# Kernel tuning notes

Measured on AMD Instinct MI355X. Metric: run time of the kernel, lower is better.

Reference implementation:

```python
import jax, jax.numpy as jnp
import numpy as np

N = 100000       # nodes
E = 800000       # edges (avg degree 8)
D_IN = 256
D_H = 128
K = 16           # cluster_num
LAMBDA1 = 1.0    # args.alphaH
LAMBDA2 = 0.5    # args.alphaO
GAMMA = 0.1      # args.step_size_gamma


def setup_inputs() -> dict:
    key = jax.random.key(0)
    ks = jax.random.split(key, 8)
    x = jax.random.normal(ks[0], (N, D_IN), jnp.float32)
    edge_index = jax.random.randint(ks[1], (2, E), 0, N, jnp.int32)
    # learned params (glorot-ish small init to keep Gram term numerically tame)
    W1 = jax.random.normal(ks[2], (D_IN, D_H), jnp.float32) * 0.002
    b1 = jnp.zeros((D_H,), jnp.float32)
    W2 = jax.random.normal(ks[3], (D_H, D_H), jnp.float32) * 0.01
    b2 = jnp.zeros((D_H,), jnp.float32)
    Wf = jax.random.normal(ks[4], (D_H, K), jnp.float32) * 0.05
    bf = jnp.zeros((K,), jnp.float32)
    return {"x": x, "edge_index": edge_index, "W1": W1, "b1": b1,
            "W2": W2, "b2": b2, "Wf": Wf, "bf": bf}


def _gcn_norm(edge_index, n):
    # add self loops, symmetric normalization D^-1/2 A D^-1/2 (PyG gcn_norm)
    loops = jnp.arange(n, dtype=edge_index.dtype)
    row = jnp.concatenate([edge_index[0], loops])   # source
    col = jnp.concatenate([edge_index[1], loops])   # target
    w = jnp.ones(row.shape[0], jnp.float32)
    deg = jax.ops.segment_sum(w, col, num_segments=n)
    dinv = jnp.where(deg > 0, jax.lax.rsqrt(jnp.maximum(deg, 1.0)), 0.0)
    return row, col, dinv[row] * w * dinv[col]


def _deprop_layer(x, W, b, row, col, w, n):
    x = x @ W                                               # lin (no bias)
    z = (1.0 - GAMMA * LAMBDA1 + GAMMA * LAMBDA2) * x
    # propagate: gather source features, scale by edge weight, scatter-add to target
    s = GAMMA * LAMBDA1 * jax.ops.segment_sum(w[:, None] * x[row], col, num_segments=n)
    # dense Gram correction: x @ (x^T x), d_h x d_h contraction
    t = GAMMA * LAMBDA2 * (x @ (x.T @ x))
    return jax.nn.relu(z + s - t + b)                       # bias add + ReLU


def reference(x, edge_index, W1, b1, W2, b2, Wf, bf):
    n = x.shape[0]
    row, col, w = _gcn_norm(edge_index, n)  # cached=True -> computed once, reused
    x = _deprop_layer(x, W1, b1, row, col, w, n)
    x = _deprop_layer(x, W2, b2, row, col, w, n)
    logits = x @ Wf + bf                    # fc; dropout is identity in eval mode
    return jax.nn.log_softmax(logits, axis=1)
```

## Files before the change

kernel.cpp:

```cpp
#include <hip/hip_runtime.h>

#define NNODES 100000
#define NEDGES 800000
#define DIN    256
#define DH     128
#define KCLS   16
#define SCAN_NBLK 98
#define GCH 64
#define GRAM_BLK 256

typedef unsigned short u16;
typedef short s16x8 __attribute__((ext_vector_type(8)));
typedef float f32x4 __attribute__((ext_vector_type(4)));

static constexpr float CZ = 0.95f;
static constexpr float CS = 0.10f;
static constexpr float CT = 0.05f;

__device__ __forceinline__ u16 f2b(float f) {
    unsigned u = __builtin_bit_cast(unsigned, f);
    return (u16)((u + 0x7FFFu + ((u >> 16) & 1u)) >> 16);
}
__device__ __forceinline__ float b2f(u16 b) {
    return __builtin_bit_cast(float, ((unsigned)b) << 16);
}
__device__ __forceinline__ s16x8 f2b8(float4 u0, float4 u1) {
    s16x8 v;
    v[0] = (short)f2b(u0.x); v[1] = (short)f2b(u0.y);
    v[2] = (short)f2b(u0.z); v[3] = (short)f2b(u0.w);
    v[4] = (short)f2b(u1.x); v[5] = (short)f2b(u1.y);
    v[6] = (short)f2b(u1.z); v[7] = (short)f2b(u1.w);
    return v;
}


__global__ __launch_bounds__(256) void zero_kernel(int* __restrict__ p) {
    int i = blockIdx.x * 256 + threadIdx.x;
    if (i < NNODES) p[i] = 0;
}

__global__ __launch_bounds__(256) void hist_kernel(const int* __restrict__ col, int* counts) {
    int i = blockIdx.x * 256 + threadIdx.x;
    if (i < NEDGES) atomicAdd(&counts[col[i]], 1);
}

__global__ __launch_bounds__(256) void dinv_kernel(const int* __restrict__ counts, float* dinv) {
    int i = blockIdx.x * 256 + threadIdx.x;
    if (i < NNODES) dinv[i] = rsqrtf((float)(counts[i] + 1));
}

__global__ __launch_bounds__(256) void scan1_kernel(const int* __restrict__ counts,
                                                    int* __restrict__ offsets, int* __restrict__ bsum) {
    __shared__ int ls[256];
    const int b = blockIdx.x, t = threadIdx.x;
    const int base = b * 1024 + t * 4;
    int v0 = (base + 0 < NNODES) ? counts[base + 0] : 0;
    int v1 = (base + 1 < NNODES) ? counts[base + 1] : 0;
    int v2 = (base + 2 < NNODES) ? counts[base + 2] : 0;
    int v3 = (base + 3 < NNODES) ? counts[base + 3] : 0;
    ls[t] = v0 + v1 + v2 + v3;
    __syncthreads();
    for (int off = 1; off < 256; off <<= 1) {
        int v = (t >= off) ? ls[t - off] : 0;
        __syncthreads();
        ls[t] += v;
        __syncthreads();
    }
    int excl = (t == 0) ? 0 : ls[t - 1];
    if (t == 255) bsum[b] = ls[255];
    if (base + 0 < NNODES) offsets[base + 0] = excl;
    if (base + 1 < NNODES) offsets[base + 1] = excl + v0;
    if (base + 2 < NNODES) offsets[base + 2] = excl + v0 + v1;
    if (base + 3 < NNODES) offsets[base + 3] = excl + v0 + v1 + v2;
}

__global__ __launch_bounds__(128) void scan2_kernel(int* bsum) {
    __shared__ int ls[128];
    const int t = threadIdx.x;
    int v = (t < SCAN_NBLK) ? bsum[t] : 0;
    ls[t] = v;
    __syncthreads();
    for (int off = 1; off < 128; off <<= 1) {
        int u = (t >= off) ? ls[t - off] : 0;
        __syncthreads();
        ls[t] += u;
        __syncthreads();
    }
    if (t < SCAN_NBLK) bsum[t] = ls[t] - v;
}

__global__ __launch_bounds__(256) void scan3_kernel(int* __restrict__ offsets, const int* __restrict__ bsum) {
    const int b = blockIdx.x, t = threadIdx.x;
    const int add = bsum[b];
    const int base = b * 1024 + t * 4;
    #pragma unroll
    for (int i = 0; i < 4; ++i)
        if (base + i < NNODES) offsets[base + i] += add;
    if (b == 0 && t == 0) offsets[NNODES] = NEDGES;
}

__global__ __launch_bounds__(256)
void fill_kernel(const int* __restrict__ row, const int* __restrict__ col,
                 const int* __restrict__ offsets, int* __restrict__ cursor,
                 int* __restrict__ eidx) {
    int e = blockIdx.x * 256 + threadIdx.x;
    if (e >= NEDGES) return;
    int c = col[e];
    int p = offsets[c] + atomicAdd(&cursor[c], 1);
    eidx[p] = row[e];
}


template<int KD>
__global__ __launch_bounds__(256)
void tr_w_kernel(const float* __restrict__ W, u16* __restrict__ Wt) {
    int idx = blockIdx.x * 256 + threadIdx.x;
    if (idx < 128 * KD) {
        int c = idx / KD, k = idx % KD;
        Wt[idx] = f2b(W[k * 128 + c]);
    }
}

template<int KD, int EPI, int AF, int WS>
__global__ __launch_bounds__(256, 4)
void mm_bt(const void* __restrict__ Avoid, const u16* __restrict__ Bt,
           u16* __restrict__ Out, const u16* __restrict__ Hb,
           const u16* __restrict__ Sb, const float* __restrict__ bias,
           const float* __restrict__ dinvp, u16* __restrict__ Hs,
           int nrows)
{
    __shared__ __align__(16) u16 as_[2][128 * 40];
    __shared__ __align__(16) u16 bs_[2][128 * 40];
    const int t = threadIdx.x;
    const int w = t >> 6, l = t & 63;
    const int l15 = l & 15, g = l >> 4;
    const int row0 = blockIdx.x * 128;

    const u16*   Ab = (const u16*)Avoid;
    const float* Af = (const float*)Avoid;

    const int sr = t >> 2, so = t & 3;
    int arow[2];
    arow[0] = min(row0 + sr,      nrows - 1);
    arow[1] = min(row0 + 64 + sr, nrows - 1);

    #pragma unroll
    for (int i = 0; i < 2; ++i) {
        s16x8 va;
        if (AF) {
            const float4* p = (const float4*)&Af[(size_t)arow[i] * KD + so * 8];
            va = f2b8(p[0], p[1]);
        } else {
            va = *(const s16x8*)&Ab[(size_t)arow[i] * KD + so * 8];
        }
        s16x8 vb = *(const s16x8*)&Bt[(size_t)(sr + i * 64) * KD + so * 8];
        *(s16x8*)&as_[0][(sr + i * 64) * 40 + so * 8] = va;
        *(s16x8*)&bs_[0][(sr + i * 64) * 40 + so * 8] = vb;
    }
    __syncthreads();

    f32x4 acc[2][8] = {};
    constexpr int NK = KD / 32;

    for (int kc = 0; kc < NK; ++kc) {
        const int buf = kc & 1;
        s16x8 va[2], vb[2];
        const bool pf = (kc + 1 < NK);
        if (pf) {
            const int k0 = (kc + 1) * 32;
            #pragma unroll
            for (int i = 0; i < 2; ++i) {
                if (AF) {
                    const float4* p = (const float4*)&Af[(size_t)arow[i] * KD + k0 + so * 8];
                    va[i] = f2b8(p[0], p[1]);
                } else {
                    va[i] = *(const s16x8*)&Ab[(size_t)arow[i] * KD + k0 + so * 8];
                }
                vb[i] = *(const s16x8*)&Bt[(size_t)(sr + i * 64) * KD + k0 + so * 8];
            }
        }
        s16x8 af0 = *(const s16x8*)&as_[buf][(w * 32 +      l15) * 40 + g * 8];
        s16x8 af1 = *(const s16x8*)&as_[buf][(w * 32 + 16 + l15) * 40 + g * 8];
        #pragma unroll
        for (int n = 0; n < 8; ++n) {
            s16x8 bfr = *(const s16x8*)&bs_[buf][(n * 16 + l15) * 40 + g * 8];
            acc[0][n] = __builtin_amdgcn_mfma_f32_16x16x32_bf16(af0, bfr, acc[0][n], 0, 0, 0);
            acc[1][n] = __builtin_amdgcn_mfma_f32_16x16x32_bf16(af1, bfr, acc[1][n], 0, 0, 0);
        }
        if (pf) {
            #pragma unroll
            for (int i = 0; i < 2; ++i) {
                *(s16x8*)&as_[buf ^ 1][(sr + i * 64) * 40 + so * 8] = va[i];
                *(s16x8*)&bs_[buf ^ 1][(sr + i * 64) * 40 + so * 8] = vb[i];
            }
        }
        __syncthreads();
    }

    float bv[8];
    if (EPI) {
        #pragma unroll
        for (int n = 0; n < 8; ++n) bv[n] = bias[n * 16 + l15];
    }
    #pragma unroll
    for (int m = 0; m < 2; ++m) {
        #pragma unroll
        for (int j = 0; j < 4; ++j) {
            int grow = row0 + w * 32 + m * 16 + g * 4 + j;
            if (grow < nrows) {
                size_t base = (size_t)grow * 128;
                float dv = WS ? dinvp[grow] : 0.f;
                #pragma unroll
                for (int n = 0; n < 8; ++n) {
                    int col = n * 16 + l15;
                    float v = acc[m][n][j];
                    if (EPI) {
                        float h = b2f(Hb[base + col]);
                        float s = b2f(Sb[base + col]);
                        v = fmaxf(CZ * h + CS * s - CT * v + bv[n], 0.f);
                    }
                    Out[base + col] = f2b(v);
                    if (WS) Hs[base + col] = f2b(dv * v);
                }
            }
        }
    }
}

__global__ __launch_bounds__(256)
void gram_gather(const u16* __restrict__ Hb, const u16* __restrict__ Hsb,
                 const float* __restrict__ dinv,
                 const int* __restrict__ offsets, const int* __restrict__ eidx,
                 float* __restrict__ P, u16* __restrict__ Sb, int nrows)
{
    __shared__ __align__(16) u16 ht[128 * GCH];
    const int t = threadIdx.x;

    if (blockIdx.x < GRAM_BLK) {
        const int bid = blockIdx.x;
        const int w = t >> 6, l = t & 63;
        const int l15 = l & 15, g = l >> 4;
        const int nch = (nrows + GCH - 1) / GCH;

        f32x4 acc[2][8] = {};
        const int sr = t >> 2, sq = t & 3;

        for (int ch = bid; ch < nch; ch += GRAM_BLK) {
            {
                int gr = ch * GCH + sr;
                #pragma unroll
                for (int i4 = 0; i4 < 4; ++i4) {
                    int c0 = sq * 32 + i4 * 8;
                    s16x8 v = {};
                    if (gr < nrows) v = *(const s16x8*)&Hb[(size_t)gr * DH + c0];
                    #pragma unroll
                    for (int i = 0; i < 8; ++i) {
                        int c = c0 + i;
                        ht[c * GCH + (sr ^ ((c & 7) << 3))] = (u16)v[i];
                    }
                }
            }
            __syncthreads();
            #pragma unroll
            for (int ks = 0; ks < 2; ++ks) {
                const int kx = (ks * 32 + g * 8) ^ ((l & 7) << 3);
                s16x8 a0 = *(const s16x8*)&ht[(w * 32 +      l15) * GCH + kx];
                s16x8 a1 = *(const s16x8*)&ht[(w * 32 + 16 + l15) * GCH + kx];
                #pragma unroll
                for (int n = 0; n < 8; ++n) {
                    s16x8 bfr = *(const s16x8*)&ht[(n * 16 + l15) * GCH + kx];
                    acc[0][n] = __builtin_amdgcn_mfma_f32_16x16x32_bf16(a0, bfr, acc[0][n], 0, 0, 0);
                    acc[1][n] = __builtin_amdgcn_mfma_f32_16x16x32_bf16(a1, bfr, acc[1][n], 0, 0, 0);
                }
            }
            __syncthreads();
        }

        float* Pb = P + (size_t)bid * (DH * DH);
        #pragma unroll
        for (int m = 0; m < 2; ++m)
            #pragma unroll
            for (int j = 0; j < 4; ++j) {
                int prow = w * 32 + m * 16 + g * 4 + j;
                #pragma unroll
                for (int n = 0; n < 8; ++n)
                    Pb[prow * DH + n * 16 + l15] = acc[m][n][j];
            }
    } else {
        const int grp = t >> 4;
        const int gl  = t & 15;
        const int node = (blockIdx.x - GRAM_BLK) * 16 + grp;
        if (node >= NNODES) return;
        const s16x8* Hs8 = (const s16x8*)Hsb;
        const float d = dinv[node];
        s16x8 hv = Hs8[(size_t)node * 16 + gl];
        float a[8];
        #pragma unroll
        for (int i = 0; i < 8; ++i) a[i] = b2f((u16)hv[i]);
        int p = offsets[node];
        const int e = offsets[node + 1];
        for (; p + 3 < e; p += 4) {
            int r0 = eidx[p], r1 = eidx[p + 1], r2 = eidx[p + 2], r3 = eidx[p + 3];
            s16x8 h0 = Hs8[(size_t)r0 * 16 + gl];
            s16x8 h1 = Hs8[(size_t)r1 * 16 + gl];
            s16x8 h2 = Hs8[(size_t)r2 * 16 + gl];
            s16x8 h3 = Hs8[(size_t)r3 * 16 + gl];
            #pragma unroll
            for (int i = 0; i < 8; ++i) a[i] += b2f((u16)h0[i]);
            #pragma unroll
            for (int i = 0; i < 8; ++i) a[i] += b2f((u16)h1[i]);
            #pragma unroll
            for (int i = 0; i < 8; ++i) a[i] += b2f((u16)h2[i]);
            #pragma unroll
            for (int i = 0; i < 8; ++i) a[i] += b2f((u16)h3[i]);
        }
        for (; p < e; ++p) {
            int r0 = eidx[p];
            s16x8 h0 = Hs8[(size_t)r0 * 16 + gl];
            #pragma unroll
            for (int i = 0; i < 8; ++i) a[i] += b2f((u16)h0[i]);
        }
        s16x8 o;
        #pragma unroll
        for (int i = 0; i < 8; ++i) o[i] = (short)f2b(d * a[i]);
        ((s16x8*)Sb)[(size_t)node * 16 + gl] = o;
    }
}

__global__ __launch_bounds__(256)
void gram_reduce(const float* __restrict__ P, u16* __restrict__ Gb) {
    int idx = blockIdx.x * 256 + threadIdx.x;
    float s = 0.f;
    #pragma unroll 8
    for (int p = 0; p < GRAM_BLK; ++p)
        s += P[(size_t)p * (DH * DH) + idx];
    Gb[idx] = f2b(s);
}

__global__ __launch_bounds__(256)
void fc_mfma(const u16* __restrict__ Xb, const float* __restrict__ Wf,
             const float* __restrict__ bf, float* __restrict__ out, int nrows)
{
    __shared__ __align__(16) u16 wt[KCLS * DH];
    const int t = threadIdx.x;
    const int w = t >> 6, l = t & 63;
    const int l15 = l & 15, g = l >> 4;
    const int row0 = blockIdx.x * 128 + w * 32;

    for (int idx = t; idx < KCLS * DH; idx += 256) {
        int c = idx >> 7, k = idx & 127;
        wt[c * DH + (k ^ ((c & 7) << 3))] = f2b(Wf[k * KCLS + c]);
    }
    __syncthreads();

    int r[2];
    r[0] = min(row0 + l15,      nrows - 1);
    r[1] = min(row0 + 16 + l15, nrows - 1);

    f32x4 acc[2] = {};
    #pragma unroll
    for (int k0 = 0; k0 < DH; k0 += 32) {
        s16x8 a0 = *(const s16x8*)&Xb[(size_t)r[0] * DH + k0 + g * 8];
        s16x8 a1 = *(const s16x8*)&Xb[(size_t)r[1] * DH + k0 + g * 8];
        s16x8 bfr = *(const s16x8*)&wt[l15 * DH + ((k0 + g * 8) ^ ((l & 7) << 3))];
        acc[0] = __builtin_amdgcn_mfma_f32_16x16x32_bf16(a0, bfr, acc[0], 0, 0, 0);
        acc[1] = __builtin_amdgcn_mfma_f32_16x16x32_bf16(a1, bfr, acc[1], 0, 0, 0);
    }

    const float bias = bf[l15];
    #pragma unroll
    for (int m = 0; m < 2; ++m) {
        #pragma unroll
        for (int j = 0; j < 4; ++j) {
            int grow = row0 + m * 16 + g * 4 + j;
            float v = acc[m][j] + bias;
            float mx = v;
            #pragma unroll
            for (int o = 8; o >= 1; o >>= 1)
                mx = fmaxf(mx, __shfl_xor(mx, o));
            float e = expf(v - mx);
            float ssum = e;
            #pragma unroll
            for (int o = 8; o >= 1; o >>= 1)
                ssum += __shfl_xor(ssum, o);
            if (grow < nrows)
                out[(size_t)grow * KCLS + l15] = v - mx - logf(ssum);
        }
    }
}

extern "C" void kernel_launch(void* const* d_in, const int* in_sizes, int n_in,
                              void* d_out, int out_size, void* d_ws, size_t ws_size,
                              hipStream_t stream) {
    const float* x  = (const float*)d_in[0];
    const int*   ei = (const int*)d_in[1];
    const float* W1 = (const float*)d_in[2];
    const float* b1 = (const float*)d_in[3];
    const float* W2 = (const float*)d_in[4];
    const float* b2 = (const float*)d_in[5];
    const float* Wf = (const float*)d_in[6];
    const float* bf = (const float*)d_in[7];
    float* out = (float*)d_out;

    const int* row = ei;
    const int* col = ei + NEDGES;

    float* dinv    = (float*)d_ws;
    float* P       = dinv + 102400;
    int*   counts  = (int*)(P + (size_t)GRAM_BLK * DH * DH);
    int*   offsets = counts + 102400;
    int*   bsum    = offsets + 102656;
    int*   eidx    = bsum + 128;
    u16*   B0b     = (u16*)(eidx + NEDGES);
    u16*   B1b     = B0b + (size_t)NNODES * DH;
    u16*   Sb      = B1b + (size_t)NNODES * DH;
    u16*   Hsb     = Sb + (size_t)NNODES * DH;
    u16*   W1t     = Hsb + (size_t)NNODES * DH;
    u16*   W2t     = W1t + 128 * DIN;
    u16*   Gb      = W2t + 128 * DH;

    dim3 b256(256);
    const int gN  = (NNODES + 255) / 256;
    const int gE  = (NEDGES + 255) / 256;
    const int gMM = (NNODES + 127) / 128;
    const int gGG = GRAM_BLK + (NNODES + 15) / 16;

    zero_kernel<<<gN, b256, 0, stream>>>(counts);
    hist_kernel<<<gE, b256, 0, stream>>>(col, counts);
    dinv_kernel<<<gN, b256, 0, stream>>>(counts, dinv);
    scan1_kernel<<<SCAN_NBLK, b256, 0, stream>>>(counts, offsets, bsum);
    scan2_kernel<<<1, 128, 0, stream>>>(bsum);
    scan3_kernel<<<SCAN_NBLK, b256, 0, stream>>>(offsets, bsum);
    zero_kernel<<<gN, b256, 0, stream>>>(counts);
    fill_kernel<<<gE, b256, 0, stream>>>(row, col, offsets, counts, eidx);
    tr_w_kernel<DIN><<<(128 * DIN + 255) / 256, b256, 0, stream>>>(W1, W1t);
    tr_w_kernel<DH><<<(128 * DH + 255) / 256, b256, 0, stream>>>(W2, W2t);

    mm_bt<DIN, 0, 1, 1><<<gMM, b256, 0, stream>>>(x, W1t, B0b, nullptr, nullptr, nullptr, dinv, Hsb, NNODES);
    gram_gather<<<gGG, b256, 0, stream>>>(B0b, Hsb, dinv, offsets, eidx, P, Sb, NNODES);
    gram_reduce<<<64, b256, 0, stream>>>(P, Gb);
    mm_bt<DH, 1, 0, 0><<<gMM, b256, 0, stream>>>(B0b, Gb, B1b, B0b, Sb, b1, nullptr, nullptr, NNODES);

    mm_bt<DH, 0, 0, 1><<<gMM, b256, 0, stream>>>(B1b, W2t, B0b, nullptr, nullptr, nullptr, dinv, Hsb, NNODES);
    gram_gather<<<gGG, b256, 0, stream>>>(B0b, Hsb, dinv, offsets, eidx, P, Sb, NNODES);
    gram_reduce<<<64, b256, 0, stream>>>(P, Gb);
    mm_bt<DH, 1, 0, 0><<<gMM, b256, 0, stream>>>(B0b, Gb, B1b, B0b, Sb, b2, nullptr, nullptr, NNODES);

    fc_mfma<<<gMM, b256, 0, stream>>>(B1b, Wf, bf, out, NNODES);
}
```

Before: 319.4 us.

## Record edge ranks during histogram and shrink matmul tiles to 64 rows

The histogram kernel now stores each edge's atomic rank, so the CSR fill no longer needs a second zeroing pass or a second round of atomics on the counters. Separately, the node-by-feature matmul drops from 128-row double-buffered tiles to 64-row single-buffered tiles, which doubles the grid and cuts shared memory per block. The fill change trades an extra 800K-int rank array write and read for removing one kernel and contended atomics. The matmul change loses prefetch overlap and B-tile reuse in exchange for more blocks and higher occupancy.

```diff
diff --git a/kernel.cpp b/kernel.cpp
--- a/kernel.cpp
+++ b/kernel.cpp
@@ -39,9 +39,11 @@
     if (i < NNODES) p[i] = 0;
 }
 
-__global__ __launch_bounds__(256) void hist_kernel(const int* __restrict__ col, int* counts) {
+__global__ __launch_bounds__(256)
+void hist_kernel(const int* __restrict__ col, int* __restrict__ counts,
+                 int* __restrict__ rank) {
     int i = blockIdx.x * 256 + threadIdx.x;
-    if (i < NEDGES) atomicAdd(&counts[col[i]], 1);
+    if (i < NEDGES) rank[i] = atomicAdd(&counts[col[i]], 1);
 }
 
 __global__ __launch_bounds__(256) void dinv_kernel(const int* __restrict__ counts, float* dinv) {
@@ -101,13 +103,11 @@
 
 __global__ __launch_bounds__(256)
 void fill_kernel(const int* __restrict__ row, const int* __restrict__ col,
-                 const int* __restrict__ offsets, int* __restrict__ cursor,
+                 const int* __restrict__ offsets, const int* __restrict__ rank,
                  int* __restrict__ eidx) {
     int e = blockIdx.x * 256 + threadIdx.x;
     if (e >= NEDGES) return;
-    int c = col[e];
-    int p = offsets[c] + atomicAdd(&cursor[c], 1);
-    eidx[p] = row[e];
+    eidx[offsets[col[e]] + rank[e]] = row[e];
 }
 
 
@@ -122,79 +122,51 @@
 }
 
 template<int KD, int EPI, int AF, int WS>
-__global__ __launch_bounds__(256, 4)
+__global__ __launch_bounds__(256)
 void mm_bt(const void* __restrict__ Avoid, const u16* __restrict__ Bt,
            u16* __restrict__ Out, const u16* __restrict__ Hb,
            const u16* __restrict__ Sb, const float* __restrict__ bias,
            const float* __restrict__ dinvp, u16* __restrict__ Hs,
            int nrows)
 {
-    __shared__ __align__(16) u16 as_[2][128 * 40];
-    __shared__ __align__(16) u16 bs_[2][128 * 40];
+    __shared__ __align__(16) u16 as_[64 * 40];
+    __shared__ __align__(16) u16 bs_[128 * 40];
     const int t = threadIdx.x;
     const int w = t >> 6, l = t & 63;
     const int l15 = l & 15, g = l >> 4;
-    const int row0 = blockIdx.x * 128;
+    const int row0 = blockIdx.x * 64;
 
     const u16*   Ab = (const u16*)Avoid;
     const float* Af = (const float*)Avoid;
 
     const int sr = t >> 2, so = t & 3;
-    int arow[2];
-    arow[0] = min(row0 + sr,      nrows - 1);
-    arow[1] = min(row0 + 64 + sr, nrows - 1);
-
-    #pragma unroll
-    for (int i = 0; i < 2; ++i) {
+    const int srow = min(row0 + sr, nrows - 1);
+
+    f32x4 acc[8] = {};
+    constexpr int NK = KD / 32;
+
+    for (int kc = 0; kc < NK; ++kc) {
+        const int k0 = kc * 32;
         s16x8 va;
         if (AF) {
-            const float4* p = (const float4*)&Af[(size_t)arow[i] * KD + so * 8];
+            const float4* p = (const float4*)&Af[(size_t)srow * KD + k0 + so * 8];
             va = f2b8(p[0], p[1]);
         } else {
-            va = *(const s16x8*)&Ab[(size_t)arow[i] * KD + so * 8];
-        }
-        s16x8 vb = *(const s16x8*)&Bt[(size_t)(sr + i * 64) * KD + so * 8];
-        *(s16x8*)&as_[0][(sr + i * 64) * 40 + so * 8] = va;
-        *(s16x8*)&bs_[0][(sr + i * 64) * 40 + so * 8] = vb;
-    }
-    __syncthreads();
-
-    f32x4 acc[2][8] = {};
-    constexpr int NK = KD / 32;
-
-    for (int kc = 0; kc < NK; ++kc) {
-        const int buf = kc & 1;
-        s16x8 va[2], vb[2];
-        const bool pf = (kc + 1 < NK);
-        if (pf) {
-            const int k0 = (kc + 1) * 32;
-            #pragma unroll
-            for (int i = 0; i < 2; ++i) {
-                if (AF) {
-                    const float4* p = (const float4*)&Af[(size_t)arow[i] * KD + k0 + so * 8];
-                    va[i] = f2b8(p[0], p[1]);
-                } else {
-                    va[i] = *(const s16x8*)&Ab[(size_t)arow[i] * KD + k0 + so * 8];
-                }
-                vb[i] = *(const s16x8*)&Bt[(size_t)(sr + i * 64) * KD + k0 + so * 8];
-            }
-        }
-        s16x8 af0 = *(const s16x8*)&as_[buf][(w * 32 +      l15) * 40 + g * 8];
-        s16x8 af1 = *(const s16x8*)&as_[buf][(w * 32 + 16 + l15) * 40 + g * 8];
+            va = *(const s16x8*)&Ab[(size_t)srow * KD + k0 + so * 8];
+        }
+        s16x8 vb0 = *(const s16x8*)&Bt[(size_t)sr        * KD + k0 + so * 8];
+        s16x8 vb1 = *(const s16x8*)&Bt[(size_t)(sr + 64) * KD + k0 + so * 8];
+        if (kc) __syncthreads();
+        *(s16x8*)&as_[sr * 40 + so * 8]        = va;
+        *(s16x8*)&bs_[sr * 40 + so * 8]        = vb0;
+        *(s16x8*)&bs_[(sr + 64) * 40 + so * 8] = vb1;
+        __syncthreads();
+        s16x8 af = *(const s16x8*)&as_[(w * 16 + l15) * 40 + g * 8];
         #pragma unroll
         for (int n = 0; n < 8; ++n) {
-            s16x8 bfr = *(const s16x8*)&bs_[buf][(n * 16 + l15) * 40 + g * 8];
-            acc[0][n] = __builtin_amdgcn_mfma_f32_16x16x32_bf16(af0, bfr, acc[0][n], 0, 0, 0);
-            acc[1][n] = __builtin_amdgcn_mfma_f32_16x16x32_bf16(af1, bfr, acc[1][n], 0, 0, 0);
-        }
-        if (pf) {
-            #pragma unroll
-            for (int i = 0; i < 2; ++i) {
-                *(s16x8*)&as_[buf ^ 1][(sr + i * 64) * 40 + so * 8] = va[i];
-                *(s16x8*)&bs_[buf ^ 1][(sr + i * 64) * 40 + so * 8] = vb[i];
-            }
-        }
-        __syncthreads();
+            s16x8 bfr = *(const s16x8*)&bs_[(n * 16 + l15) * 40 + g * 8];
+            acc[n] = __builtin_amdgcn_mfma_f32_16x16x32_bf16(af, bfr, acc[n], 0, 0, 0);
+        }
     }
 
     float bv[8];
@@ -203,25 +175,22 @@
         for (int n = 0; n < 8; ++n) bv[n] = bias[n * 16 + l15];
     }
     #pragma unroll
-    for (int m = 0; m < 2; ++m) {
-        #pragma unroll
-        for (int j = 0; j < 4; ++j) {
-            int grow = row0 + w * 32 + m * 16 + g * 4 + j;
-            if (grow < nrows) {
-                size_t base = (size_t)grow * 128;
-                float dv = WS ? dinvp[grow] : 0.f;
-                #pragma unroll
-                for (int n = 0; n < 8; ++n) {
-                    int col = n * 16 + l15;
-                    float v = acc[m][n][j];
-                    if (EPI) {
-                        float h = b2f(Hb[base + col]);
-                        float s = b2f(Sb[base + col]);
-                        v = fmaxf(CZ * h + CS * s - CT * v + bv[n], 0.f);
-                    }
-                    Out[base + col] = f2b(v);
-                    if (WS) Hs[base + col] = f2b(dv * v);
+    for (int j = 0; j < 4; ++j) {
+        int grow = row0 + w * 16 + g * 4 + j;
+        if (grow < nrows) {
+            size_t base = (size_t)grow * 128;
+            float dv = WS ? dinvp[grow] : 0.f;
+            #pragma unroll
+            for (int n = 0; n < 8; ++n) {
+                int col = n * 16 + l15;
+                float v = acc[n][j];
+                if (EPI) {
+                    float h = b2f(Hb[base + col]);
+                    float s = b2f(Sb[base + col]);
+                    v = fmaxf(CZ * h + CS * s - CT * v + bv[n], 0.f);
                 }
+                Out[base + col] = f2b(v);
+                if (WS) Hs[base + col] = f2b(dv * v);
             }
         }
     }
@@ -411,7 +380,8 @@
     int*   offsets = counts + 102400;
     int*   bsum    = offsets + 102656;
     int*   eidx    = bsum + 128;
-    u16*   B0b     = (u16*)(eidx + NEDGES);
+    int*   rank    = eidx + NEDGES;
+    u16*   B0b     = (u16*)(rank + NEDGES);
     u16*   B1b     = B0b + (size_t)NNODES * DH;
     u16*   Sb      = B1b + (size_t)NNODES * DH;
     u16*   Hsb     = Sb + (size_t)NNODES * DH;
@@ -420,19 +390,19 @@
     u16*   Gb      = W2t + 128 * DH;
 
     dim3 b256(256);
-    const int gN  = (NNODES + 255) / 256;
-    const int gE  = (NEDGES + 255) / 256;
-    const int gMM = (NNODES + 127) / 128;
-    const int gGG = GRAM_BLK + (NNODES + 15) / 16;
+    const int gN   = (NNODES + 255) / 256;
+    const int gE   = (NEDGES + 255) / 256;
+    const int gMM  = (NNODES + 63) / 64;
+    const int gFC  = (NNODES + 127) / 128;
+    const int gGG  = GRAM_BLK + (NNODES + 15) / 16;
 
     zero_kernel<<<gN, b256, 0, stream>>>(counts);
-    hist_kernel<<<gE, b256, 0, stream>>>(col, counts);
+    hist_kernel<<<gE, b256, 0, stream>>>(col, counts, rank);
     dinv_kernel<<<gN, b256, 0, stream>>>(counts, dinv);
     scan1_kernel<<<SCAN_NBLK, b256, 0, stream>>>(counts, offsets, bsum);
     scan2_kernel<<<1, 128, 0, stream>>>(bsum);
     scan3_kernel<<<SCAN_NBLK, b256, 0, stream>>>(offsets, bsum);
-    zero_kernel<<<gN, b256, 0, stream>>>(counts);
-    fill_kernel<<<gE, b256, 0, stream>>>(row, col, offsets, counts, eidx);
+    fill_kernel<<<gE, b256, 0, stream>>>(row, col, offsets, rank, eidx);
     tr_w_kernel<DIN><<<(128 * DIN + 255) / 256, b256, 0, stream>>>(W1, W1t);
     tr_w_kernel<DH><<<(128 * DH + 255) / 256, b256, 0, stream>>>(W2, W2t);
 
@@ -446,5 +416,5 @@
     gram_reduce<<<64, b256, 0, stream>>>(P, Gb);
     mm_bt<DH, 1, 0, 0><<<gMM, b256, 0, stream>>>(B0b, Gb, B1b, B0b, Sb, b2, nullptr, nullptr, NNODES);
 
-    fc_mfma<<<gMM, b256, 0, stream>>>(B1b, Wf, bf, out, NNODES);
-}
+    fc_mfma<<<gFC, b256, 0, stream>>>(B1b, Wf, bf, out, NNODES);
+}
```

Result: faster. 282.0 us, median of 2 (-11.7%).
